# Kernel optimization log

Hardware: AMD Instinct MI355X
Metric: run time of the kernel (lower is better)

Reference implementation:

```python
import jax, jax.numpy as jnp
import numpy as np

N_NODES = 100000
N_EDGES = 3200000
N_FEAT = 64
HIDDEN = 20
N_CLASSES = 10
BN_EPS = 1e-5


def _lin_init(key, fan_in, fan_out):
    k1, k2 = jax.random.split(key)
    bound = 1.0 / np.sqrt(fan_in)
    W = jax.random.uniform(k1, (fan_in, fan_out), jnp.float32, -bound, bound)
    b = jax.random.uniform(k2, (fan_out,), jnp.float32, -bound, bound)
    return W, b


def setup_inputs() -> dict:
    key = jax.random.key(0)
    ks = jax.random.split(key, 12)
    x = jax.random.normal(ks[0], (N_NODES, N_FEAT), jnp.float32)
    edge_index = jax.random.randint(ks[1], (2, N_EDGES), 0, N_NODES, jnp.int32)
    edge_weights = jax.random.uniform(ks[2], (N_EDGES,), jnp.float32)
    w1a, b1a = _lin_init(ks[3], N_FEAT, HIDDEN)
    w2a, b2a = _lin_init(ks[4], HIDDEN, HIDDEN)
    w1b, b1b = _lin_init(ks[5], HIDDEN, HIDDEN)
    w2b, b2b = _lin_init(ks[6], HIDDEN, HIDDEN)
    w1c, b1c = _lin_init(ks[7], HIDDEN, HIDDEN)
    w2c, b2c = _lin_init(ks[8], HIDDEN, HIDDEN)
    wlin, blin = _lin_init(ks[9], 3 * HIDDEN, N_CLASSES)
    g1 = jnp.ones((HIDDEN,), jnp.float32); be1 = jnp.zeros((HIDDEN,), jnp.float32)
    g2 = jnp.ones((HIDDEN,), jnp.float32); be2 = jnp.zeros((HIDDEN,), jnp.float32)
    return {
        'x': x, 'edge_index': edge_index, 'edge_weights': edge_weights,
        'w1a': w1a, 'b1a': b1a, 'w2a': w2a, 'b2a': b2a, 'g1': g1, 'be1': be1,
        'w1b': w1b, 'b1b': b1b, 'w2b': w2b, 'b2b': b2b, 'g2': g2, 'be2': be2,
        'w1c': w1c, 'b1c': b1c, 'w2c': w2c, 'b2c': b2c,
        'wlin': wlin, 'blin': blin,
    }


def _gin_conv(h, src, dst, w, W1, b1, W2, b2):
    # gather source node features, scale per-edge, scatter-add at destination
    m = h[src] * w[:, None]                                  # [E, d]
    agg = jax.ops.segment_sum(m, dst, num_segments=N_NODES)  # [N, d]
    z = jax.nn.relu(agg @ W1 + b1)
    return jax.nn.relu(z @ W2 + b2)


def _bn(h, gamma, beta):
    mu = jnp.mean(h, axis=0)
    var = jnp.var(h, axis=0)
    return gamma * (h - mu) * jax.lax.rsqrt(var + BN_EPS) + beta


def reference(x, edge_index, edge_weights,
              w1a, b1a, w2a, b2a, g1, be1,
              w1b, b1b, w2b, b2b, g2, be2,
              w1c, b1c, w2c, b2c, wlin, blin):
    src, dst = edge_index[0], edge_index[1]
    o1 = _gin_conv(x, src, dst, edge_weights, w1a, b1a, w2a, b2a)
    o1 = _bn(jax.nn.relu(o1), g1, be1)
    o2 = _gin_conv(o1, src, dst, edge_weights, w1b, b1b, w2b, b2b)
    o2 = _bn(jax.nn.relu(o2), g2, be2)
    o3 = jax.nn.relu(_gin_conv(o2, src, dst, edge_weights, w1c, b1c, w2c, b2c))
    emb = jnp.concatenate([o1, o2, o3], axis=1)  # [N, 60]
    return emb @ wlin + blin
```

## Files before the change

kernel.cpp:

```cpp
#include <hip/hip_runtime.h>
#include <hip/hip_fp16.h>

#define N_NODES 100000
#define N_EDGES 3200000
#define N_FEAT  64
#define HIDDEN  20
#define N_CLASSES 10
#define BN_EPS  1e-5f
#define NPB     51
#define NREG    391
#define RCAP    10240
#define RCAP2   12288
#define TILE    4096
#define NTILE   ((N_EDGES + TILE - 1) / TILE)
#define EPT     16
#define WSCALE  (1.0f / 32767.0f)
#define YSTRIDE 32

__device__ __forceinline__ void fma4h(float4& acc, float s, float2 raw) {
    const __half2* h = (const __half2*)&raw;
    float2 a = __half22float2(h[0]);
    float2 b = __half22float2(h[1]);
    acc.x += s * a.x; acc.y += s * a.y; acc.z += s * b.x; acc.w += s * b.y;
}

__global__ __launch_bounds__(256) void partition_kernel(const int* __restrict__ ei,
                                                        const float* __restrict__ ew,
                                                        int* __restrict__ rcur,
                                                        int2* __restrict__ staging) {
    __shared__ int hist[NREG];
    __shared__ int base[NREG];
    int tid = threadIdx.x;
    for (int r = tid; r < NREG; r += 256) hist[r] = 0;
    __syncthreads();

    int t0 = blockIdx.x * TILE;
    int2 ebuf[EPT];
    int  rbuf[EPT];
    #pragma unroll
    for (int k = 0; k < EPT; ++k) {
        int i = t0 + tid + k * 256;
        if (i < N_EDGES) {
            int src = ei[i];
            int dst = ei[N_EDGES + i];
            float w = ew[i];
            int r = dst >> 8;
            ebuf[k].x = src | ((dst & 255) << 17);
            ebuf[k].y = __float_as_int(w);
            rbuf[k] = r;
            atomicAdd(&hist[r], 1);
        } else {
            rbuf[k] = -1;
        }
    }
    __syncthreads();

    for (int r = tid; r < NREG; r += 256) {
        int c = hist[r];
        base[r] = (c > 0) ? atomicAdd(&rcur[r], c) : 0;
        hist[r] = 0;
    }
    __syncthreads();

    #pragma unroll
    for (int k = 0; k < EPT; ++k) {
        int r = rbuf[k];
        if (r >= 0) {
            int rank = atomicAdd(&hist[r], 1);
            int p = base[r] + rank;
            if (p < RCAP) staging[(size_t)r * RCAP + p] = ebuf[k];
        }
    }
}

__global__ __launch_bounds__(256) void region_kernel(const int* __restrict__ rcur,
                                                     const int2* __restrict__ staging,
                                                     int* __restrict__ rowstart,
                                                     int* __restrict__ nbatch,
                                                     int* __restrict__ edges) {
    __shared__ int h[256];
    __shared__ int s[256];
    int tid = threadIdx.x;
    int r = blockIdx.x;
    int cnt = min(rcur[r], RCAP);
    const int2* sg = staging + (size_t)r * RCAP;

    h[tid] = 0;
    __syncthreads();
    for (int i = tid; i < cnt; i += 256)
        atomicAdd(&h[(sg[i].x >> 17) & 255], 1);
    __syncthreads();

    int v = h[tid];
    int p = (v + 7) & ~7;
    s[tid] = p;
    __syncthreads();
    for (int off = 1; off < 256; off <<= 1) {
        int u = (tid >= off) ? s[tid - off] : 0;
        __syncthreads();
        s[tid] += u;
        __syncthreads();
    }
    int start = r * RCAP2 + (s[tid] - p);
    int node = (r << 8) + tid;
    if (node < N_NODES) {
        rowstart[node] = start;
        nbatch[node] = p >> 3;
    }
    h[tid] = start;
    __syncthreads();

    for (int i = tid; i < cnt; i += 256) {
        int2 e = sg[i];
        int dl = (e.x >> 17) & 255;
        int wq = __float2int_rn(__int_as_float(e.y) * 32767.0f);
        wq = min(max(wq, 0), 32767);
        int pos = atomicAdd(&h[dl], 1);
        edges[pos] = (e.x & 0x1FFFF) | (wq << 17);
    }
    __syncthreads();
    for (int j = start + v; j < start + p; ++j) edges[j] = 0;
}

__global__ __launch_bounds__(256) void pre1_kernel(const float* __restrict__ x,
                                                   const float* __restrict__ W1,
                                                   __half* __restrict__ y) {
    __shared__ float sW[N_FEAT * HIDDEN];
    __shared__ float sx[NPB * 65];
    int tid = threadIdx.x;
    for (int i = tid; i < N_FEAT * HIDDEN; i += 256) sW[i] = W1[i];
    int base = blockIdx.x * NPB;
    int nrows = min(NPB, N_NODES - base);
    int total = nrows * N_FEAT;
    const float* xb = x + (size_t)base * N_FEAT;
    for (int i = tid; i < total; i += 256) {
        int r = i >> 6, c = i & 63;
        sx[r * 65 + c] = xb[i];
    }
    __syncthreads();

    int n_local = tid / 5;
    int q = tid - n_local * 5;
    int n = base + n_local;
    if (tid >= 255 || n >= N_NODES) return;

    float a0 = 0.f, a1 = 0.f, a2 = 0.f, a3 = 0.f;
    const float* row = &sx[n_local * 65];
    const float* wq = &sW[4 * q];
    #pragma unroll
    for (int k = 0; k < N_FEAT; ++k) {
        float xv = row[k];
        a0 += xv * wq[k * HIDDEN + 0];
        a1 += xv * wq[k * HIDDEN + 1];
        a2 += xv * wq[k * HIDDEN + 2];
        a3 += xv * wq[k * HIDDEN + 3];
    }
    float2 st;
    ((__half2*)&st)[0] = __floats2half2_rn(a0, a1);
    ((__half2*)&st)[1] = __floats2half2_rn(a2, a3);
    *(float2*)(y + (size_t)n * YSTRIDE + 4 * q) = st;
}

template <bool STATS, bool FINAL>
__global__ __launch_bounds__(512) void gin_fused(const int* __restrict__ rowstart,
                                                 const int* __restrict__ nbatch,
                                                 const int* __restrict__ edges,
                                                 const __half* __restrict__ y,
                                                 const float* __restrict__ b1,
                                                 const float* __restrict__ W2,
                                                 const float* __restrict__ b2,
                                                 float* __restrict__ opre,
                                                 float* __restrict__ stats,
                                                 const float* __restrict__ o1bn,
                                                 const float* __restrict__ o2bn,
                                                 const float* __restrict__ wlin,
                                                 const float* __restrict__ blin,
                                                 float* __restrict__ out) {
    __shared__ float sW2[HIDDEN * HIDDEN];
    __shared__ float sb1[HIDDEN];
    __shared__ float sb2[HIDDEN];
    __shared__ float zsh[NPB * HIDDEN];
    __shared__ float psh[NPB * HIDDEN];
    __shared__ float sstat[STATS ? 2 * HIDDEN : 1];
    __shared__ float sfin[FINAL ? (2 * NPB * HIDDEN + 3 * HIDDEN * N_CLASSES + N_CLASSES) : 1];

    int tid = threadIdx.x;
    for (int i = tid; i < HIDDEN * HIDDEN; i += 512) sW2[i] = W2[i];
    if (tid < HIDDEN) { sb1[tid] = b1[tid]; sb2[tid] = b2[tid]; }
    if (STATS) {
        if (tid < 2 * HIDDEN) sstat[tid] = 0.f;
    }
    float* osh1 = sfin;
    float* osh2 = sfin + NPB * HIDDEN;
    float* sw   = sfin + 2 * NPB * HIDDEN;
    float* sb   = sw + 3 * HIDDEN * N_CLASSES;
    if (FINAL) {
        for (int i = tid; i < 3 * HIDDEN * N_CLASSES; i += 512) sw[i] = wlin[i];
        if (tid < N_CLASSES) sb[tid] = blin[tid];
    }
    __syncthreads();

    int n_local = tid / 10;
    int sub = tid - n_local * 10;
    int q = sub % 5;
    int g = sub / 5;
    int n = blockIdx.x * NPB + n_local;
    bool act = (tid < 510) && (n < N_NODES);

    const __half* ybase = y + 4 * q;

    float4 acc0 = make_float4(0.f, 0.f, 0.f, 0.f);
    float4 acc1 = acc0, acc2 = acc0, acc3 = acc0;
    if (act) {
        int s0 = rowstart[n];
        int nb = nbatch[n];
        int bh = (nb + 1) >> 1;
        int b0 = g ? bh : 0;
        int b1 = g ? nb : bh;
        for (int b = b0; b < b1; ++b) {
            const int* ep = edges + s0 + b * 8;
            int4 ea = *(const int4*)ep;
            int4 eb = *(const int4*)(ep + 4);
            float2 v0 = *(const float2*)(ybase + ((size_t)(ea.x & 0x1FFFF) << 5));
            float2 v1 = *(const float2*)(ybase + ((size_t)(ea.y & 0x1FFFF) << 5));
            float2 v2 = *(const float2*)(ybase + ((size_t)(ea.z & 0x1FFFF) << 5));
            float2 v3 = *(const float2*)(ybase + ((size_t)(ea.w & 0x1FFFF) << 5));
            float2 v4 = *(const float2*)(ybase + ((size_t)(eb.x & 0x1FFFF) << 5));
            float2 v5 = *(const float2*)(ybase + ((size_t)(eb.y & 0x1FFFF) << 5));
            float2 v6 = *(const float2*)(ybase + ((size_t)(eb.z & 0x1FFFF) << 5));
            float2 v7 = *(const float2*)(ybase + ((size_t)(eb.w & 0x1FFFF) << 5));
            fma4h(acc0, (float)((unsigned)ea.x >> 17) * WSCALE, v0);
            fma4h(acc1, (float)((unsigned)ea.y >> 17) * WSCALE, v1);
            fma4h(acc2, (float)((unsigned)ea.z >> 17) * WSCALE, v2);
            fma4h(acc3, (float)((unsigned)ea.w >> 17) * WSCALE, v3);
            fma4h(acc0, (float)((unsigned)eb.x >> 17) * WSCALE, v4);
            fma4h(acc1, (float)((unsigned)eb.y >> 17) * WSCALE, v5);
            fma4h(acc2, (float)((unsigned)eb.z >> 17) * WSCALE, v6);
            fma4h(acc3, (float)((unsigned)eb.w >> 17) * WSCALE, v7);
        }
    }
    acc0.x += acc1.x + acc2.x + acc3.x;
    acc0.y += acc1.y + acc2.y + acc3.y;
    acc0.z += acc1.z + acc2.z + acc3.z;
    acc0.w += acc1.w + acc2.w + acc3.w;

    if (act && g == 1) {
        float* pr = &psh[n_local * HIDDEN + 4 * q];
        pr[0] = acc0.x; pr[1] = acc0.y; pr[2] = acc0.z; pr[3] = acc0.w;
    }
    __syncthreads();
    if (act && g == 0) {
        const float* pr = &psh[n_local * HIDDEN + 4 * q];
        float* zr = &zsh[n_local * HIDDEN + 4 * q];
        zr[0] = fmaxf(acc0.x + pr[0] + sb1[4 * q + 0], 0.f);
        zr[1] = fmaxf(acc0.y + pr[1] + sb1[4 * q + 1], 0.f);
        zr[2] = fmaxf(acc0.z + pr[2] + sb1[4 * q + 2], 0.f);
        zr[3] = fmaxf(acc0.w + pr[3] + sb1[4 * q + 3], 0.f);
    }
    __syncthreads();

    float o[4] = {0.f, 0.f, 0.f, 0.f};
    bool lead = act && (g == 0);
    if (lead) {
        o[0] = sb2[4 * q + 0]; o[1] = sb2[4 * q + 1];
        o[2] = sb2[4 * q + 2]; o[3] = sb2[4 * q + 3];
        const float* zr = &zsh[n_local * HIDDEN];
        const float* wq = &sW2[4 * q];
        #pragma unroll
        for (int k = 0; k < HIDDEN; ++k) {
            float zk = zr[k];
            o[0] += zk * wq[k * HIDDEN + 0];
            o[1] += zk * wq[k * HIDDEN + 1];
            o[2] += zk * wq[k * HIDDEN + 2];
            o[3] += zk * wq[k * HIDDEN + 3];
        }
        #pragma unroll
        for (int j = 0; j < 4; ++j) o[j] = fmaxf(o[j], 0.f);
        if (!FINAL) {
            float* wr = opre + (size_t)n * HIDDEN + 4 * q;
            *(float4*)wr = make_float4(o[0], o[1], o[2], o[3]);
        }
    }

    if (STATS) {
        if (lead) {
            #pragma unroll
            for (int j = 0; j < 4; ++j) {
                atomicAdd(&sstat[4 * q + j], o[j]);
                atomicAdd(&sstat[HIDDEN + 4 * q + j], o[j] * o[j]);
            }
        }
        __syncthreads();
        if (tid < 2 * HIDDEN) atomicAdd(&stats[tid], sstat[tid]);
    }

    if (FINAL) {
        __syncthreads();
        if (lead) {
            float* zr = &zsh[n_local * HIDDEN + 4 * q];
            zr[0] = o[0]; zr[1] = o[1]; zr[2] = o[2]; zr[3] = o[3];
            float4 v1 = *(const float4*)(o1bn + (size_t)n * HIDDEN + 4 * q);
            float4 v2 = *(const float4*)(o2bn + (size_t)n * HIDDEN + 4 * q);
            float* p1 = &osh1[n_local * HIDDEN + 4 * q];
            float* p2 = &osh2[n_local * HIDDEN + 4 * q];
            p1[0] = v1.x; p1[1] = v1.y; p1[2] = v1.z; p1[3] = v1.w;
            p2[0] = v2.x; p2[1] = v2.y; p2[2] = v2.z; p2[3] = v2.w;
        }
        __syncthreads();
        if (lead) {
            int c = 2 * q;
            float a0 = sb[c], a1 = sb[c + 1];
            const float* r1 = &osh1[n_local * HIDDEN];
            const float* r2 = &osh2[n_local * HIDDEN];
            const float* r3 = &zsh[n_local * HIDDEN];
            #pragma unroll
            for (int j = 0; j < HIDDEN; ++j) {
                float v = r1[j];
                a0 += v * sw[j * N_CLASSES + c];
                a1 += v * sw[j * N_CLASSES + c + 1];
            }
            #pragma unroll
            for (int j = 0; j < HIDDEN; ++j) {
                float v = r2[j];
                a0 += v * sw[(HIDDEN + j) * N_CLASSES + c];
                a1 += v * sw[(HIDDEN + j) * N_CLASSES + c + 1];
            }
            #pragma unroll
            for (int j = 0; j < HIDDEN; ++j) {
                float v = r3[j];
                a0 += v * sw[(2 * HIDDEN + j) * N_CLASSES + c];
                a1 += v * sw[(2 * HIDDEN + j) * N_CLASSES + c + 1];
            }
            float* wr = out + (size_t)n * N_CLASSES + c;
            wr[0] = a0; wr[1] = a1;
        }
    }
}

__global__ __launch_bounds__(256) void bn_fuse(const float* __restrict__ opre,
                                               const float* __restrict__ stats,
                                               const float* __restrict__ gamma,
                                               const float* __restrict__ beta,
                                               float* __restrict__ obn,
                                               const float* __restrict__ Wnext,
                                               __half* __restrict__ y) {
    __shared__ float sc[HIDDEN], sh[HIDDEN];
    __shared__ float sW[HIDDEN * HIDDEN];
    __shared__ float hsh[NPB * HIDDEN];
    int tid = threadIdx.x;
    for (int i = tid; i < HIDDEN * HIDDEN; i += 256) sW[i] = Wnext[i];
    if (tid < HIDDEN) {
        const float invN = 1.0f / N_NODES;
        float mu  = stats[tid] * invN;
        float var = stats[HIDDEN + tid] * invN - mu * mu;
        float inv = rsqrtf(var + BN_EPS);
        float s = gamma[tid] * inv;
        sc[tid] = s;
        sh[tid] = beta[tid] - mu * s;
    }
    __syncthreads();

    int n_local = tid / 5;
    int q = tid - n_local * 5;
    int n = blockIdx.x * NPB + n_local;
    bool act = (tid < 255) && (n < N_NODES);

    if (act) {
        float4 v = *(const float4*)(opre + (size_t)n * HIDDEN + 4 * q);
        float h0 = v.x * sc[4 * q + 0] + sh[4 * q + 0];
        float h1 = v.y * sc[4 * q + 1] + sh[4 * q + 1];
        float h2 = v.z * sc[4 * q + 2] + sh[4 * q + 2];
        float h3 = v.w * sc[4 * q + 3] + sh[4 * q + 3];
        *(float4*)(obn + (size_t)n * HIDDEN + 4 * q) = make_float4(h0, h1, h2, h3);
        float* hr = &hsh[n_local * HIDDEN + 4 * q];
        hr[0] = h0; hr[1] = h1; hr[2] = h2; hr[3] = h3;
    }
    __syncthreads();

    if (act) {
        float a0 = 0.f, a1 = 0.f, a2 = 0.f, a3 = 0.f;
        const float* hr = &hsh[n_local * HIDDEN];
        const float* wq = &sW[4 * q];
        #pragma unroll
        for (int k = 0; k < HIDDEN; ++k) {
            float hk = hr[k];
            a0 += hk * wq[k * HIDDEN + 0];
            a1 += hk * wq[k * HIDDEN + 1];
            a2 += hk * wq[k * HIDDEN + 2];
            a3 += hk * wq[k * HIDDEN + 3];
        }
        float2 st;
        ((__half2*)&st)[0] = __floats2half2_rn(a0, a1);
        ((__half2*)&st)[1] = __floats2half2_rn(a2, a3);
        *(float2*)(y + (size_t)n * YSTRIDE + 4 * q) = st;
    }
}

extern "C" void kernel_launch(void* const* d_in, const int* in_sizes, int n_in,
                              void* d_out, int out_size, void* d_ws, size_t ws_size,
                              hipStream_t stream) {
    const float* x   = (const float*)d_in[0];
    const int*   ei  = (const int*)d_in[1];
    const float* ew  = (const float*)d_in[2];
    const float* w1a = (const float*)d_in[3];
    const float* b1a = (const float*)d_in[4];
    const float* w2a = (const float*)d_in[5];
    const float* b2a = (const float*)d_in[6];
    const float* g1  = (const float*)d_in[7];
    const float* be1 = (const float*)d_in[8];
    const float* w1b = (const float*)d_in[9];
    const float* b1b = (const float*)d_in[10];
    const float* w2b = (const float*)d_in[11];
    const float* b2b = (const float*)d_in[12];
    const float* g2  = (const float*)d_in[13];
    const float* be2 = (const float*)d_in[14];
    const float* w1c = (const float*)d_in[15];
    const float* b1c = (const float*)d_in[16];
    const float* w2c = (const float*)d_in[17];
    const float* b2c = (const float*)d_in[18];
    const float* wlin = (const float*)d_in[19];
    const float* blin = (const float*)d_in[20];
    float* out = (float*)d_out;

    char* base = (char*)d_ws;
    size_t ob = 0;
    int* rcur = (int*)(base + ob);      ob += NREG * 4;
    float* st1 = (float*)(base + ob);   ob += 2 * HIDDEN * 4;
    float* st2 = (float*)(base + ob);   ob += 2 * HIDDEN * 4;
    const size_t zero_bytes = ob;
    int* rowstart = (int*)(base + ob);  ob += N_NODES * 4;
    int* nbatch   = (int*)(base + ob);  ob += N_NODES * 4;
    ob = (ob + 63) & ~(size_t)63;
    int* edges = (int*)(base + ob);     ob += (size_t)NREG * RCAP2 * 4;
    ob = (ob + 63) & ~(size_t)63;
    const size_t u0 = ob;
    int2* staging = (int2*)(base + u0);
    __half* y   = (__half*)(base + u0);
    float* opre = (float*)(base + u0 + 6400000);
    float* o1bn = (float*)(base + u0 + 14400000);
    float* o2bn = (float*)(base + u0 + 22400000);

    const int fusedBlocks = (N_NODES + NPB - 1) / NPB;

    (void)hipMemsetAsync(base, 0, zero_bytes, stream);
    partition_kernel<<<NTILE, 256, 0, stream>>>(ei, ew, rcur, staging);
    region_kernel<<<NREG, 256, 0, stream>>>(rcur, staging, rowstart, nbatch, edges);

    pre1_kernel<<<fusedBlocks, 256, 0, stream>>>(x, w1a, y);
    gin_fused<true, false><<<fusedBlocks, 512, 0, stream>>>(
        rowstart, nbatch, edges, y, b1a, w2a, b2a, opre, st1,
        o1bn, o2bn, wlin, blin, out);
    bn_fuse<<<fusedBlocks, 256, 0, stream>>>(opre, st1, g1, be1, o1bn, w1b, y);

    gin_fused<true, false><<<fusedBlocks, 512, 0, stream>>>(
        rowstart, nbatch, edges, y, b1b, w2b, b2b, opre, st2,
        o1bn, o2bn, wlin, blin, out);
    bn_fuse<<<fusedBlocks, 256, 0, stream>>>(opre, st2, g2, be2, o2bn, w1c, y);

    gin_fused<false, true><<<fusedBlocks, 512, 0, stream>>>(
        rowstart, nbatch, edges, y, b1c, w2c, b2c, opre, st1,
        o1bn, o2bn, wlin, blin, out);
}
```

Baseline: 279.2 us.

## Shrink half-precision feature rows to 48 bytes and gather 16-byte vectors

```diff
diff --git a/kernel.cpp b/kernel.cpp
--- a/kernel.cpp
+++ b/kernel.cpp
@@ -7,7 +7,8 @@
 #define HIDDEN  20
 #define N_CLASSES 10
 #define BN_EPS  1e-5f
-#define NPB     51
+#define PNPB    51
+#define GNPB    85
 #define NREG    391
 #define RCAP    10240
 #define RCAP2   12288
@@ -15,13 +16,16 @@
 #define NTILE   ((N_EDGES + TILE - 1) / TILE)
 #define EPT     16
 #define WSCALE  (1.0f / 32767.0f)
-#define YSTRIDE 32
-
-__device__ __forceinline__ void fma4h(float4& acc, float s, float2 raw) {
+#define YSTRIDE 24
+
+__device__ __forceinline__ void fma8h(float4& lo, float4& hi, float s, const float4& raw) {
     const __half2* h = (const __half2*)&raw;
     float2 a = __half22float2(h[0]);
     float2 b = __half22float2(h[1]);
-    acc.x += s * a.x; acc.y += s * a.y; acc.z += s * b.x; acc.w += s * b.y;
+    float2 c = __half22float2(h[2]);
+    float2 d = __half22float2(h[3]);
+    lo.x += s * a.x; lo.y += s * a.y; lo.z += s * b.x; lo.w += s * b.y;
+    hi.x += s * c.x; hi.y += s * c.y; hi.z += s * d.x; hi.w += s * d.y;
 }
 
 __global__ __launch_bounds__(256) void partition_kernel(const int* __restrict__ ei,
@@ -119,18 +123,18 @@
         edges[pos] = (e.x & 0x1FFFF) | (wq << 17);
     }
     __syncthreads();
-    for (int j = start + v; j < start + p; ++j) edges[j] = 0;
+    for (int jj = start + v; jj < start + p; ++jj) edges[jj] = 0;
 }
 
 __global__ __launch_bounds__(256) void pre1_kernel(const float* __restrict__ x,
                                                    const float* __restrict__ W1,
                                                    __half* __restrict__ y) {
     __shared__ float sW[N_FEAT * HIDDEN];
-    __shared__ float sx[NPB * 65];
+    __shared__ float sx[PNPB * 65];
     int tid = threadIdx.x;
     for (int i = tid; i < N_FEAT * HIDDEN; i += 256) sW[i] = W1[i];
-    int base = blockIdx.x * NPB;
-    int nrows = min(NPB, N_NODES - base);
+    int base = blockIdx.x * PNPB;
+    int nrows = min(PNPB, N_NODES - base);
     int total = nrows * N_FEAT;
     const float* xb = x + (size_t)base * N_FEAT;
     for (int i = tid; i < total; i += 256) {
@@ -155,10 +159,20 @@
         a2 += xv * wq[k * HIDDEN + 2];
         a3 += xv * wq[k * HIDDEN + 3];
     }
-    float2 st;
-    ((__half2*)&st)[0] = __floats2half2_rn(a0, a1);
-    ((__half2*)&st)[1] = __floats2half2_rn(a2, a3);
-    *(float2*)(y + (size_t)n * YSTRIDE + 4 * q) = st;
+    if (q < 4) {
+        float2 st;
+        ((__half2*)&st)[0] = __floats2half2_rn(a0, a1);
+        ((__half2*)&st)[1] = __floats2half2_rn(a2, a3);
+        *(float2*)(y + (size_t)n * YSTRIDE + 4 * q) = st;
+    } else {
+        float4 st4;
+        __half2* hp = (__half2*)&st4;
+        hp[0] = __floats2half2_rn(a0, a1);
+        hp[1] = __floats2half2_rn(a2, a3);
+        hp[2] = __floats2half2_rn(0.f, 0.f);
+        hp[3] = __floats2half2_rn(0.f, 0.f);
+        *(float4*)(y + (size_t)n * YSTRIDE + 16) = st4;
+    }
 }
 
 template <bool STATS, bool FINAL>
@@ -176,13 +190,13 @@
                                                  const float* __restrict__ wlin,
                                                  const float* __restrict__ blin,
                                                  float* __restrict__ out) {
+    __shared__ float pbuf[2 * GNPB * 24];
+    __shared__ float zsh[GNPB * HIDDEN];
     __shared__ float sW2[HIDDEN * HIDDEN];
     __shared__ float sb1[HIDDEN];
     __shared__ float sb2[HIDDEN];
-    __shared__ float zsh[NPB * HIDDEN];
-    __shared__ float psh[NPB * HIDDEN];
     __shared__ float sstat[STATS ? 2 * HIDDEN : 1];
-    __shared__ float sfin[FINAL ? (2 * NPB * HIDDEN + 3 * HIDDEN * N_CLASSES + N_CLASSES) : 1];
+    __shared__ float swl[FINAL ? (3 * HIDDEN * N_CLASSES + N_CLASSES) : 1];
 
     int tid = threadIdx.x;
     for (int i = tid; i < HIDDEN * HIDDEN; i += 512) sW2[i] = W2[i];
@@ -190,81 +204,87 @@
     if (STATS) {
         if (tid < 2 * HIDDEN) sstat[tid] = 0.f;
     }
-    float* osh1 = sfin;
-    float* osh2 = sfin + NPB * HIDDEN;
-    float* sw   = sfin + 2 * NPB * HIDDEN;
-    float* sb   = sw + 3 * HIDDEN * N_CLASSES;
+    float* sw = swl;
+    float* sb = swl + 3 * HIDDEN * N_CLASSES;
     if (FINAL) {
         for (int i = tid; i < 3 * HIDDEN * N_CLASSES; i += 512) sw[i] = wlin[i];
         if (tid < N_CLASSES) sb[tid] = blin[tid];
     }
     __syncthreads();
 
-    int n_local = tid / 10;
-    int sub = tid - n_local * 10;
-    int q = sub % 5;
-    int g = sub / 5;
-    int n = blockIdx.x * NPB + n_local;
-    bool act = (tid < 510) && (n < N_NODES);
-
-    const __half* ybase = y + 4 * q;
-
-    float4 acc0 = make_float4(0.f, 0.f, 0.f, 0.f);
-    float4 acc1 = acc0, acc2 = acc0, acc3 = acc0;
-    if (act) {
-        int s0 = rowstart[n];
-        int nb = nbatch[n];
-        int bh = (nb + 1) >> 1;
-        int b0 = g ? bh : 0;
-        int b1 = g ? nb : bh;
-        for (int b = b0; b < b1; ++b) {
-            const int* ep = edges + s0 + b * 8;
-            int4 ea = *(const int4*)ep;
-            int4 eb = *(const int4*)(ep + 4);
-            float2 v0 = *(const float2*)(ybase + ((size_t)(ea.x & 0x1FFFF) << 5));
-            float2 v1 = *(const float2*)(ybase + ((size_t)(ea.y & 0x1FFFF) << 5));
-            float2 v2 = *(const float2*)(ybase + ((size_t)(ea.z & 0x1FFFF) << 5));
-            float2 v3 = *(const float2*)(ybase + ((size_t)(ea.w & 0x1FFFF) << 5));
-            float2 v4 = *(const float2*)(ybase + ((size_t)(eb.x & 0x1FFFF) << 5));
-            float2 v5 = *(const float2*)(ybase + ((size_t)(eb.y & 0x1FFFF) << 5));
-            float2 v6 = *(const float2*)(ybase + ((size_t)(eb.z & 0x1FFFF) << 5));
-            float2 v7 = *(const float2*)(ybase + ((size_t)(eb.w & 0x1FFFF) << 5));
-            fma4h(acc0, (float)((unsigned)ea.x >> 17) * WSCALE, v0);
-            fma4h(acc1, (float)((unsigned)ea.y >> 17) * WSCALE, v1);
-            fma4h(acc2, (float)((unsigned)ea.z >> 17) * WSCALE, v2);
-            fma4h(acc3, (float)((unsigned)ea.w >> 17) * WSCALE, v3);
-            fma4h(acc0, (float)((unsigned)eb.x >> 17) * WSCALE, v4);
-            fma4h(acc1, (float)((unsigned)eb.y >> 17) * WSCALE, v5);
-            fma4h(acc2, (float)((unsigned)eb.z >> 17) * WSCALE, v6);
-            fma4h(acc3, (float)((unsigned)eb.w >> 17) * WSCALE, v7);
-        }
-    }
-    acc0.x += acc1.x + acc2.x + acc3.x;
-    acc0.y += acc1.y + acc2.y + acc3.y;
-    acc0.z += acc1.z + acc2.z + acc3.z;
-    acc0.w += acc1.w + acc2.w + acc3.w;
-
-    if (act && g == 1) {
-        float* pr = &psh[n_local * HIDDEN + 4 * q];
-        pr[0] = acc0.x; pr[1] = acc0.y; pr[2] = acc0.z; pr[3] = acc0.w;
-    }
-    __syncthreads();
-    if (act && g == 0) {
-        const float* pr = &psh[n_local * HIDDEN + 4 * q];
-        float* zr = &zsh[n_local * HIDDEN + 4 * q];
-        zr[0] = fmaxf(acc0.x + pr[0] + sb1[4 * q + 0], 0.f);
-        zr[1] = fmaxf(acc0.y + pr[1] + sb1[4 * q + 1], 0.f);
-        zr[2] = fmaxf(acc0.z + pr[2] + sb1[4 * q + 2], 0.f);
-        zr[3] = fmaxf(acc0.w + pr[3] + sb1[4 * q + 3], 0.f);
+    {
+        int n_local = tid / 6;
+        int sub = tid - n_local * 6;
+        int j = sub % 3;
+        int g = sub / 3;
+        int n = blockIdx.x * GNPB + n_local;
+        bool act = (tid < 510) && (n < N_NODES);
+
+        const __half* ybase = y + 8 * j;
+        float4 a0l = make_float4(0.f, 0.f, 0.f, 0.f);
+        float4 a0h = a0l, a1l = a0l, a1h = a0l;
+
+        if (act) {
+            int s0 = rowstart[n];
+            int nb = nbatch[n];
+            int bh = (nb + 1) >> 1;
+            int b0 = g ? bh : 0;
+            int b1e = g ? nb : bh;
+            for (int b = b0; b < b1e; ++b) {
+                const int* ep = edges + s0 + b * 8;
+                int4 ea = *(const int4*)ep;
+                int4 eb = *(const int4*)(ep + 4);
+                float4 v0 = *(const float4*)(ybase + (size_t)(ea.x & 0x1FFFF) * YSTRIDE);
+                float4 v1 = *(const float4*)(ybase + (size_t)(ea.y & 0x1FFFF) * YSTRIDE);
+                float4 v2 = *(const float4*)(ybase + (size_t)(ea.z & 0x1FFFF) * YSTRIDE);
+                float4 v3 = *(const float4*)(ybase + (size_t)(ea.w & 0x1FFFF) * YSTRIDE);
+                float4 v4 = *(const float4*)(ybase + (size_t)(eb.x & 0x1FFFF) * YSTRIDE);
+                float4 v5 = *(const float4*)(ybase + (size_t)(eb.y & 0x1FFFF) * YSTRIDE);
+                float4 v6 = *(const float4*)(ybase + (size_t)(eb.z & 0x1FFFF) * YSTRIDE);
+                float4 v7 = *(const float4*)(ybase + (size_t)(eb.w & 0x1FFFF) * YSTRIDE);
+                fma8h(a0l, a0h, (float)((unsigned)ea.x >> 17) * WSCALE, v0);
+                fma8h(a1l, a1h, (float)((unsigned)ea.y >> 17) * WSCALE, v1);
+                fma8h(a0l, a0h, (float)((unsigned)ea.z >> 17) * WSCALE, v2);
+                fma8h(a1l, a1h, (float)((unsigned)ea.w >> 17) * WSCALE, v3);
+                fma8h(a0l, a0h, (float)((unsigned)eb.x >> 17) * WSCALE, v4);
+                fma8h(a1l, a1h, (float)((unsigned)eb.y >> 17) * WSCALE, v5);
+                fma8h(a0l, a0h, (float)((unsigned)eb.z >> 17) * WSCALE, v6);
+                fma8h(a1l, a1h, (float)((unsigned)eb.w >> 17) * WSCALE, v7);
+            }
+        }
+        a0l.x += a1l.x; a0l.y += a1l.y; a0l.z += a1l.z; a0l.w += a1l.w;
+        a0h.x += a1h.x; a0h.y += a1h.y; a0h.z += a1h.z; a0h.w += a1h.w;
+
+        if (act) {
+            float* pr = &pbuf[(g * GNPB + n_local) * 24 + 8 * j];
+            *(float4*)pr = a0l;
+            *((float4*)pr + 1) = a0h;
+        }
+    }
+    __syncthreads();
+
+    int nl = tid / 5;
+    int q = tid - nl * 5;
+    int n = blockIdx.x * GNPB + nl;
+    bool act5 = (tid < 5 * GNPB) && (n < N_NODES);
+
+    if (act5) {
+        const float* za = &pbuf[nl * 24];
+        const float* zb = &pbuf[(GNPB + nl) * 24];
+        float* zr = &zsh[nl * HIDDEN + 4 * q];
+        #pragma unroll
+        for (int i = 0; i < 4; ++i) {
+            int f = 4 * q + i;
+            zr[i] = fmaxf(za[f] + zb[f] + sb1[f], 0.f);
+        }
     }
     __syncthreads();
 
     float o[4] = {0.f, 0.f, 0.f, 0.f};
-    bool lead = act && (g == 0);
-    if (lead) {
+    if (act5) {
         o[0] = sb2[4 * q + 0]; o[1] = sb2[4 * q + 1];
         o[2] = sb2[4 * q + 2]; o[3] = sb2[4 * q + 3];
-        const float* zr = &zsh[n_local * HIDDEN];
+        const float* zr = &zsh[nl * HIDDEN];
         const float* wq = &sW2[4 * q];
         #pragma unroll
         for (int k = 0; k < HIDDEN; ++k) {
@@ -275,7 +295,7 @@
             o[3] += zk * wq[k * HIDDEN + 3];
         }
         #pragma unroll
-        for (int j = 0; j < 4; ++j) o[j] = fmaxf(o[j], 0.f);
+        for (int j2 = 0; j2 < 4; ++j2) o[j2] = fmaxf(o[j2], 0.f);
         if (!FINAL) {
             float* wr = opre + (size_t)n * HIDDEN + 4 * q;
             *(float4*)wr = make_float4(o[0], o[1], o[2], o[3]);
@@ -283,11 +303,11 @@
     }
 
     if (STATS) {
-        if (lead) {
+        if (act5) {
             #pragma unroll
-            for (int j = 0; j < 4; ++j) {
-                atomicAdd(&sstat[4 * q + j], o[j]);
-                atomicAdd(&sstat[HIDDEN + 4 * q + j], o[j] * o[j]);
+            for (int j2 = 0; j2 < 4; ++j2) {
+                atomicAdd(&sstat[4 * q + j2], o[j2]);
+                atomicAdd(&sstat[HIDDEN + 4 * q + j2], o[j2] * o[j2]);
             }
         }
         __syncthreads();
@@ -296,40 +316,42 @@
 
     if (FINAL) {
         __syncthreads();
-        if (lead) {
-            float* zr = &zsh[n_local * HIDDEN + 4 * q];
+        float* osh1 = pbuf;
+        float* osh2 = pbuf + GNPB * HIDDEN;
+        if (act5) {
+            float* zr = &zsh[nl * HIDDEN + 4 * q];
             zr[0] = o[0]; zr[1] = o[1]; zr[2] = o[2]; zr[3] = o[3];
             float4 v1 = *(const float4*)(o1bn + (size_t)n * HIDDEN + 4 * q);
             float4 v2 = *(const float4*)(o2bn + (size_t)n * HIDDEN + 4 * q);
-            float* p1 = &osh1[n_local * HIDDEN + 4 * q];
-            float* p2 = &osh2[n_local * HIDDEN + 4 * q];
+            float* p1 = &osh1[nl * HIDDEN + 4 * q];
+            float* p2 = &osh2[nl * HIDDEN + 4 * q];
             p1[0] = v1.x; p1[1] = v1.y; p1[2] = v1.z; p1[3] = v1.w;
             p2[0] = v2.x; p2[1] = v2.y; p2[2] = v2.z; p2[3] = v2.w;
         }
         __syncthreads();
-        if (lead) {
+        if (act5) {
             int c = 2 * q;
             float a0 = sb[c], a1 = sb[c + 1];
-            const float* r1 = &osh1[n_local * HIDDEN];
-            const float* r2 = &osh2[n_local * HIDDEN];
-            const float* r3 = &zsh[n_local * HIDDEN];
+            const float* r1 = &osh1[nl * HIDDEN];
+            const float* r2 = &osh2[nl * HIDDEN];
+            const float* r3 = &zsh[nl * HIDDEN];
             #pragma unroll
-            for (int j = 0; j < HIDDEN; ++j) {
-                float v = r1[j];
-                a0 += v * sw[j * N_CLASSES + c];
-                a1 += v * sw[j * N_CLASSES + c + 1];
+            for (int j2 = 0; j2 < HIDDEN; ++j2) {
+                float v = r1[j2];
+                a0 += v * sw[j2 * N_CLASSES + c];
+                a1 += v * sw[j2 * N_CLASSES + c + 1];
             }
             #pragma unroll
-            for (int j = 0; j < HIDDEN; ++j) {
-                float v = r2[j];
-                a0 += v * sw[(HIDDEN + j) * N_CLASSES + c];
-                a1 += v * sw[(HIDDEN + j) * N_CLASSES + c + 1];
+            for (int j2 = 0; j2 < HIDDEN; ++j2) {
+                float v = r2[j2];
+                a0 += v * sw[(HIDDEN + j2) * N_CLASSES + c];
+                a1 += v * sw[(HIDDEN + j2) * N_CLASSES + c + 1];
             }
             #pragma unroll
-            for (int j = 0; j < HIDDEN; ++j) {
-                float v = r3[j];
-                a0 += v * sw[(2 * HIDDEN + j) * N_CLASSES + c];
-                a1 += v * sw[(2 * HIDDEN + j) * N_CLASSES + c + 1];
+            for (int j2 = 0; j2 < HIDDEN; ++j2) {
+                float v = r3[j2];
+                a0 += v * sw[(2 * HIDDEN + j2) * N_CLASSES + c];
+                a1 += v * sw[(2 * HIDDEN + j2) * N_CLASSES + c + 1];
             }
             float* wr = out + (size_t)n * N_CLASSES + c;
             wr[0] = a0; wr[1] = a1;
@@ -346,7 +368,7 @@
                                                __half* __restrict__ y) {
     __shared__ float sc[HIDDEN], sh[HIDDEN];
     __shared__ float sW[HIDDEN * HIDDEN];
-    __shared__ float hsh[NPB * HIDDEN];
+    __shared__ float hsh[PNPB * HIDDEN];
     int tid = threadIdx.x;
     for (int i = tid; i < HIDDEN * HIDDEN; i += 256) sW[i] = Wnext[i];
     if (tid < HIDDEN) {
@@ -362,7 +384,7 @@
 
     int n_local = tid / 5;
     int q = tid - n_local * 5;
-    int n = blockIdx.x * NPB + n_local;
+    int n = blockIdx.x * PNPB + n_local;
     bool act = (tid < 255) && (n < N_NODES);
 
     if (act) {
@@ -436,28 +458,29 @@
     const size_t u0 = ob;
     int2* staging = (int2*)(base + u0);
     __half* y   = (__half*)(base + u0);
-    float* opre = (float*)(base + u0 + 6400000);
-    float* o1bn = (float*)(base + u0 + 14400000);
-    float* o2bn = (float*)(base + u0 + 22400000);
-
-    const int fusedBlocks = (N_NODES + NPB - 1) / NPB;
+    float* opre = (float*)(base + u0 + 4800000);
+    float* o1bn = (float*)(base + u0 + 12800000);
+    float* o2bn = (float*)(base + u0 + 20800000);
+
+    const int preBlocks  = (N_NODES + PNPB - 1) / PNPB;
+    const int gatBlocks  = (N_NODES + GNPB - 1) / GNPB;
 
     (void)hipMemsetAsync(base, 0, zero_bytes, stream);
     partition_kernel<<<NTILE, 256, 0, stream>>>(ei, ew, rcur, staging);
     region_kernel<<<NREG, 256, 0, stream>>>(rcur, staging, rowstart, nbatch, edges);
 
-    pre1_kernel<<<fusedBlocks, 256, 0, stream>>>(x, w1a, y);
-    gin_fused<true, false><<<fusedBlocks, 512, 0, stream>>>(
+    pre1_kernel<<<preBlocks, 256, 0, stream>>>(x, w1a, y);
+    gin_fused<true, false><<<gatBlocks, 512, 0, stream>>>(
         rowstart, nbatch, edges, y, b1a, w2a, b2a, opre, st1,
         o1bn, o2bn, wlin, blin, out);
-    bn_fuse<<<fusedBlocks, 256, 0, stream>>>(opre, st1, g1, be1, o1bn, w1b, y);
-
-    gin_fused<true, false><<<fusedBlocks, 512, 0, stream>>>(
+    bn_fuse<<<preBlocks, 256, 0, stream>>>(opre, st1, g1, be1, o1bn, w1b, y);
+
+    gin_fused<true, false><<<gatBlocks, 512, 0, stream>>>(
         rowstart, nbatch, edges, y, b1b, w2b, b2b, opre, st2,
         o1bn, o2bn, wlin, blin, out);
-    bn_fuse<<<fusedBlocks, 256, 0, stream>>>(opre, st2, g2, be2, o2bn, w1c, y);
-
-    gin_fused<false, true><<<fusedBlocks, 512, 0, stream>>>(
+    bn_fuse<<<preBlocks, 256, 0, stream>>>(opre, st2, g2, be2, o2bn, w1c, y);
+
+    gin_fused<false, true><<<gatBlocks, 512, 0, stream>>>(
         rowstart, nbatch, edges, y, b1c, w2c, b2c, opre, st1,
         o1bn, o2bn, wlin, blin, out);
 }
```

Result: faster. 260.7 us (-6.6%).
